# Performance work log

Measured on AMD Instinct MI355X. Metric: run time of the kernel, lower is better.

## Reference

```python
import jax, jax.numpy as jnp
import numpy as np

B, S, D, M, K = 2, 1024, 512, 64, 4


def setup_inputs() -> dict:
    key = jax.random.key(0)
    ks = jax.random.split(key, 16)
    sd = 1.0 / np.sqrt(D)
    return {
        "x": jax.random.normal(ks[0], (B, S, D), jnp.float32),
        "context": jax.random.normal(ks[1], (B, S, D), jnp.float32),
        # per-mechanism transform Linear(d, d): weight [m, d_in, d_out], bias [m, d]
        "W_t": jax.random.normal(ks[2], (M, D, D), jnp.float32) * sd,
        "b_t": jax.random.normal(ks[3], (M, D), jnp.float32) * sd,
        # characteristics parameter (1,1,dim) per mechanism -> [m, d]
        "char": jax.random.normal(ks[4], (M, D), jnp.float32),
        # timing gate Linear(d, 1): weight [m, d], bias [m]
        "W_g": jax.random.normal(ks[5], (M, D), jnp.float32) * sd,
        "b_g": jax.random.normal(ks[6], (M,), jnp.float32) * sd,
        # selector: Linear(d, 2d) -> GELU -> Linear(2d, m)
        "sel_W1": jax.random.normal(ks[7], (D, 2 * D), jnp.float32) * sd,
        "sel_b1": jax.random.normal(ks[8], (2 * D,), jnp.float32) * sd,
        "sel_W2": jax.random.normal(ks[9], (2 * D, M), jnp.float32) / np.sqrt(2 * D),
        "sel_b2": jax.random.normal(ks[10], (M,), jnp.float32) / np.sqrt(2 * D),
        # integrate: Linear(2d, d)
        "int_W": jax.random.normal(ks[11], (2 * D, D), jnp.float32) / np.sqrt(2 * D),
        "int_b": jax.random.normal(ks[12], (D,), jnp.float32) / np.sqrt(2 * D),
    }


def reference(x, context, W_t, b_t, char, W_g, b_g, sel_W1, sel_b1, sel_W2, sel_b2, int_W, int_b):
    # router: softmax -> top-k mask -> renormalize
    h = jax.nn.gelu(context @ sel_W1 + sel_b1, approximate=False)  # [b,s,2d]
    scores = jax.nn.softmax(h @ sel_W2 + sel_b2, axis=-1)          # [b,s,m]
    _, top_idx = jax.lax.top_k(scores, K)                          # [b,s,k]
    mask = jnp.sum(jax.nn.one_hot(top_idx, M, dtype=scores.dtype), axis=-2)  # [b,s,m]
    scores = scores * mask
    scores = scores / jnp.sum(scores, axis=-1, keepdims=True)

    # dense expert compute: transform + characteristics, sigmoid timing gate
    trans = jnp.einsum('bsd,mde->bsme', x, W_t) + b_t + char       # [b,s,m,d]
    gate = jax.nn.sigmoid(jnp.einsum('bsd,md->bsm', x, W_g) + b_g)  # [b,s,m]

    # weighted combine (gate fused into routing weights)
    selected = jnp.einsum('bsme,bsm->bse', trans, scores * gate)   # [b,s,d]

    integrated = jnp.concatenate([x, selected], axis=-1) @ int_W + int_b
    return integrated
```

## Files before the change

### kernel.cpp

```cpp
#include <hip/hip_runtime.h>
#include <hip/hip_bf16.h>

#define T_TOK 2048
#define D_    512
#define TWO_D 1024
#define M_    64

typedef float  f32x4  __attribute__((ext_vector_type(4)));
typedef __bf16 bf16x8 __attribute__((ext_vector_type(8)));

__device__ __forceinline__ ushort f2bf(float f) {
    union { __hip_bfloat16 h; ushort u; } cv;
    cv.h = __float2bfloat16(f);
    return cv.u;
}
__device__ __forceinline__ float bf2f(ushort u) {
    union { unsigned int i; float f; } c; c.i = ((unsigned int)u) << 16; return c.f;
}

__device__ __forceinline__ void gl16(const void* g, void* l) {
    __builtin_amdgcn_global_load_lds(
        (const __attribute__((address_space(1))) unsigned int*)g,
        (__attribute__((address_space(3))) unsigned int*)l, 16, 0, 0);
}

__global__ __launch_bounds__(256) void k_prep(const float* __restrict__ x,
                                              const float* __restrict__ ctx,
                                              ushort* __restrict__ xs,
                                              ushort* __restrict__ cH,
                                              ushort* __restrict__ cL) {
    int b = blockIdx.x;
    int idx = (b & 1023) * 256 + threadIdx.x;
    if (b < 1024) {
        int e4  = idx * 4;
        int t   = e4 >> 9;
        int d   = e4 & 511;
        float4 v = *reinterpret_cast<const float4*>(x + e4);
        ushort4 o;
        o.x = f2bf(v.x); o.y = f2bf(v.y); o.z = f2bf(v.z); o.w = f2bf(v.w);
        *reinterpret_cast<ushort4*>(xs + (size_t)t * TWO_D + d) = o;
    } else {
        float4 v = *reinterpret_cast<const float4*>(ctx + (size_t)idx * 4);
        ushort4 h, l;
        h.x = f2bf(v.x); l.x = f2bf(v.x - bf2f(h.x));
        h.y = f2bf(v.y); l.y = f2bf(v.y - bf2f(h.y));
        h.z = f2bf(v.z); l.z = f2bf(v.z - bf2f(h.z));
        h.w = f2bf(v.w); l.w = f2bf(v.w - bf2f(h.w));
        *reinterpret_cast<ushort4*>(cH + (size_t)idx * 4) = h;
        *reinterpret_cast<ushort4*>(cL + (size_t)idx * 4) = l;
    }
}

__global__ __launch_bounds__(256) void k_split_w1t(const float* __restrict__ W1,
                                                   ushort* __restrict__ w1th,
                                                   ushort* __restrict__ w1tl) {
    int t  = threadIdx.x;
    int n  = blockIdx.x * 64 + (t >> 2);
    int kb = blockIdx.y * 64 + (t & 3) * 16;
#pragma unroll
    for (int j = 0; j < 16; j += 4) {
        ushort hh[4], ll[4];
#pragma unroll
        for (int i = 0; i < 4; i++) {
            float v = W1[(size_t)(kb + j + i) * TWO_D + n];
            ushort h = f2bf(v);
            hh[i] = h;
            ll[i] = f2bf(v - bf2f(h));
        }
        ushort4 h4, l4;
        h4.x = hh[0]; h4.y = hh[1]; h4.z = hh[2]; h4.w = hh[3];
        l4.x = ll[0]; l4.y = ll[1]; l4.z = ll[2]; l4.w = ll[3];
        *reinterpret_cast<ushort4*>(&w1th[(size_t)n * D_ + kb + j]) = h4;
        *reinterpret_cast<ushort4*>(&w1tl[(size_t)n * D_ + kb + j]) = l4;
    }
}

__global__ __launch_bounds__(256) void k_gemm1s(const ushort* __restrict__ cH,
                                                const ushort* __restrict__ cL,
                                                const ushort* __restrict__ w1th,
                                                const ushort* __restrict__ w1tl,
                                                const float* __restrict__ b1,
                                                float* __restrict__ H) {
    int col0 = blockIdx.x * 64, r0 = blockIdx.y * 64;
    __shared__ ushort sAH[2 * 4096], sAL[2 * 4096];
    __shared__ ushort sBH[2 * 4096], sBL[2 * 4096];
    int t = threadIdx.x, lane = t & 63, wave = t >> 6;
    int wm = wave >> 1, wn = wave & 1;
    int lr = lane & 15, kq = lane >> 4;

    const ushort* srcAH = cH  + (size_t)(r0  + (t >> 3)) * D_ + (t & 7) * 8;
    const ushort* srcAL = cL  + (size_t)(r0  + (t >> 3)) * D_ + (t & 7) * 8;
    const ushort* srcBH = w1th + (size_t)(col0 + (t >> 3)) * D_ + (t & 7) * 8;
    const ushort* srcBL = w1tl + (size_t)(col0 + (t >> 3)) * D_ + (t & 7) * 8;
    int r2 = (256 + t) >> 3, p2 = ((256 + t) & 7) * 8;
    const ushort* srcAH2 = cH  + (size_t)(r0  + r2) * D_ + p2;
    const ushort* srcAL2 = cL  + (size_t)(r0  + r2) * D_ + p2;
    const ushort* srcBH2 = w1th + (size_t)(col0 + r2) * D_ + p2;
    const ushort* srcBL2 = w1tl + (size_t)(col0 + r2) * D_ + p2;

    f32x4 acc[2][2];
#pragma unroll
    for (int i = 0; i < 2; i++)
#pragma unroll
        for (int j = 0; j < 2; j++)
#pragma unroll
            for (int r = 0; r < 4; r++) acc[i][j][r] = 0.0f;

    gl16(srcAH, &sAH[0] + t * 8);  gl16(srcAH2, &sAH[0] + 2048 + t * 8);
    gl16(srcAL, &sAL[0] + t * 8);  gl16(srcAL2, &sAL[0] + 2048 + t * 8);
    gl16(srcBH, &sBH[0] + t * 8);  gl16(srcBH2, &sBH[0] + 2048 + t * 8);
    gl16(srcBL, &sBL[0] + t * 8);  gl16(srcBL2, &sBL[0] + 2048 + t * 8);
    __syncthreads();

    int cur = 0;
    for (int k0 = 0; k0 < D_; k0 += 64) {
        int nxt = cur ^ 1;
        if (k0 + 64 < D_) {
            int kn = k0 + 64;
            gl16(srcAH + kn, &sAH[nxt * 4096] + t * 8);  gl16(srcAH2 + kn, &sAH[nxt * 4096] + 2048 + t * 8);
            gl16(srcAL + kn, &sAL[nxt * 4096] + t * 8);  gl16(srcAL2 + kn, &sAL[nxt * 4096] + 2048 + t * 8);
            gl16(srcBH + kn, &sBH[nxt * 4096] + t * 8);  gl16(srcBH2 + kn, &sBH[nxt * 4096] + 2048 + t * 8);
            gl16(srcBL + kn, &sBL[nxt * 4096] + t * 8);  gl16(srcBL2 + kn, &sBL[nxt * 4096] + 2048 + t * 8);
        }
#pragma unroll
        for (int kc = 0; kc < 2; kc++) {
            bf16x8 ah[2], al[2], bh[2], bl[2];
#pragma unroll
            for (int i = 0; i < 2; i++) {
                int off = cur * 4096 + (wm * 32 + i * 16 + lr) * 64 + kc * 32 + kq * 8;
                ah[i] = *reinterpret_cast<const bf16x8*>(&sAH[off]);
                al[i] = *reinterpret_cast<const bf16x8*>(&sAL[off]);
            }
#pragma unroll
            for (int j = 0; j < 2; j++) {
                int off = cur * 4096 + (wn * 32 + j * 16 + lr) * 64 + kc * 32 + kq * 8;
                bh[j] = *reinterpret_cast<const bf16x8*>(&sBH[off]);
                bl[j] = *reinterpret_cast<const bf16x8*>(&sBL[off]);
            }
#pragma unroll
            for (int i = 0; i < 2; i++)
#pragma unroll
                for (int j = 0; j < 2; j++) {
                    acc[i][j] = __builtin_amdgcn_mfma_f32_16x16x32_bf16(ah[i], bh[j], acc[i][j], 0, 0, 0);
                    acc[i][j] = __builtin_amdgcn_mfma_f32_16x16x32_bf16(ah[i], bl[j], acc[i][j], 0, 0, 0);
                    acc[i][j] = __builtin_amdgcn_mfma_f32_16x16x32_bf16(al[i], bh[j], acc[i][j], 0, 0, 0);
                }
        }
        __syncthreads();
        cur = nxt;
    }

#pragma unroll
    for (int i = 0; i < 2; i++)
#pragma unroll
        for (int j = 0; j < 2; j++) {
            int col = col0 + wn * 32 + j * 16 + lr;
            float bb = b1[col];
#pragma unroll
            for (int r = 0; r < 4; r++) {
                int row = r0 + wm * 32 + i * 16 + kq * 4 + r;
                float v = acc[i][j][r] + bb;
                H[(size_t)row * TWO_D + col] = 0.5f * v * (1.0f + erff(v * 0.70710678118654752f));
            }
        }
}

__global__ __launch_bounds__(256) void k_logits(const float* __restrict__ H,
                                                const float* __restrict__ x,
                                                const float* __restrict__ W2,
                                                const float* __restrict__ Wg,
                                                float* __restrict__ partial) {
    __shared__ float sa[64][36];
    __shared__ float sb[32][64];
    int tx = threadIdx.x & 15, ty = threadIdx.x >> 4;
    int cx = blockIdx.x;
    int row0 = blockIdx.y * 64;

    const float* Asrc; int lda, koff;
    if (cx < 8) { Asrc = H; lda = TWO_D; koff = cx * 128; }
    else        { Asrc = x; lda = D_;    koff = (cx - 8) * 128; }

    float acc[4][4];
#pragma unroll
    for (int i = 0; i < 4; i++)
#pragma unroll
        for (int j = 0; j < 4; j++) acc[i][j] = 0.0f;

    for (int k0 = 0; k0 < 128; k0 += 32) {
#pragma unroll
        for (int q = 0; q < 2; q++) {
            int f = threadIdx.x * 2 + q;
            int r = f >> 3, c = (f & 7) * 4;
            *reinterpret_cast<float4*>(&sa[r][c]) =
                *reinterpret_cast<const float4*>(&Asrc[(size_t)(row0 + r) * lda + koff + k0 + c]);
            if (cx < 8) {
                int kk = f >> 4, n4 = (f & 15) * 4;
                *reinterpret_cast<float4*>(&sb[kk][n4]) =
                    *reinterpret_cast<const float4*>(&W2[(size_t)(koff + k0 + kk) * M_ + n4]);
            } else {
                int m = f >> 3, kq = f & 7;
                float4 v2 = *reinterpret_cast<const float4*>(&Wg[(size_t)m * D_ + koff + k0 + kq * 4]);
                sb[kq * 4 + 0][m] = v2.x; sb[kq * 4 + 1][m] = v2.y;
                sb[kq * 4 + 2][m] = v2.z; sb[kq * 4 + 3][m] = v2.w;
            }
        }
        __syncthreads();
#pragma unroll
        for (int kk = 0; kk < 32; kk++) {
            float a0 = sa[ty * 4 + 0][kk], a1 = sa[ty * 4 + 1][kk];
            float a2 = sa[ty * 4 + 2][kk], a3 = sa[ty * 4 + 3][kk];
            float4 b4 = *reinterpret_cast<float4*>(&sb[kk][tx * 4]);
            acc[0][0] += a0 * b4.x; acc[0][1] += a0 * b4.y; acc[0][2] += a0 * b4.z; acc[0][3] += a0 * b4.w;
            acc[1][0] += a1 * b4.x; acc[1][1] += a1 * b4.y; acc[1][2] += a1 * b4.z; acc[1][3] += a1 * b4.w;
            acc[2][0] += a2 * b4.x; acc[2][1] += a2 * b4.y; acc[2][2] += a2 * b4.z; acc[2][3] += a2 * b4.w;
            acc[3][0] += a3 * b4.x; acc[3][1] += a3 * b4.y; acc[3][2] += a3 * b4.z; acc[3][3] += a3 * b4.w;
        }
        __syncthreads();
    }
#pragma unroll
    for (int i = 0; i < 4; i++) {
        int row = row0 + ty * 4 + i;
        float4 o;
        float* oc = reinterpret_cast<float*>(&o);
#pragma unroll
        for (int j = 0; j < 4; j++) oc[j] = acc[i][j];
        *reinterpret_cast<float4*>(&partial[((size_t)cx * T_TOK + row) * M_ + tx * 4]) = o;
    }
}

__global__ __launch_bounds__(256) void k_topk(const float* __restrict__ partial,
                                              const float* __restrict__ b2,
                                              const float* __restrict__ bg,
                                              int* __restrict__ tope,
                                              float* __restrict__ topw) {
    int t = threadIdx.x;
    int wave = t >> 6, lane = t & 63;
    int tok = blockIdx.x * 4 + wave;

    float l = b2[lane];
#pragma unroll
    for (int c = 0; c < 8; c++)
        l += partial[((size_t)c * T_TOK + tok) * M_ + lane];
    float g = bg[lane];
#pragma unroll
    for (int c = 8; c < 12; c++)
        g += partial[((size_t)c * T_TOK + tok) * M_ + lane];

    float mx = l;
#pragma unroll
    for (int off = 1; off < 64; off <<= 1) mx = fmaxf(mx, __shfl_xor(mx, off));
    float ev = expf(l - mx);
    float s = ev;
#pragma unroll
    for (int off = 1; off < 64; off <<= 1) s += __shfl_xor(s, off);
    float p = ev / s;

    float pm = p;
    int bi0, bi1, bi2, bi3; float bv0, bv1, bv2, bv3;
#pragma unroll
    for (int k = 0; k < 4; k++) {
        float bv = pm; int bi = lane;
#pragma unroll
        for (int off = 1; off < 64; off <<= 1) {
            float ov = __shfl_xor(bv, off);
            int   oi = __shfl_xor(bi, off);
            if (ov > bv || (ov == bv && oi < bi)) { bv = ov; bi = oi; }
        }
        if (k == 0) { bi0 = bi; bv0 = bv; }
        else if (k == 1) { bi1 = bi; bv1 = bv; }
        else if (k == 2) { bi2 = bi; bv2 = bv; }
        else { bi3 = bi; bv3 = bv; }
        if (lane == bi) pm = -1.0f;
    }
    float sum4 = bv0 + bv1 + bv2 + bv3;
    int   esel = (lane == 0) ? bi0 : (lane == 1) ? bi1 : (lane == 2) ? bi2 : bi3;
    float pv   = (lane == 0) ? bv0 : (lane == 1) ? bv1 : (lane == 2) ? bv2 : bv3;
    float gv = __shfl(g, esel);
    if (lane < 4) {
        float gate = 1.0f / (1.0f + expf(-gv));
        tope[tok * 4 + lane] = esel;
        topw[tok * 4 + lane] = (pv / sum4) * gate;
    }
}

__global__ __launch_bounds__(256) void k_bucket(const int* __restrict__ tope,
                                                const float* __restrict__ topw,
                                                int* __restrict__ counts,
                                                int* __restrict__ bslot,
                                                float* __restrict__ bw) {
    int e = blockIdx.x;
    int t = threadIdx.x, lane = t & 63, wave = t >> 6;
    __shared__ int s_wsum[4];
    __shared__ int s_base;
    if (t == 0) s_base = 0;

    for (int it = 0; it < 8; it++) {
        int base = it * 1024 + t * 4;
        int4 ev = *reinterpret_cast<const int4*>(tope + base);
        bool m0 = (ev.x == e), m1 = (ev.y == e), m2 = (ev.z == e), m3 = (ev.w == e);
        unsigned long long b0 = __ballot(m0), b1 = __ballot(m1);
        unsigned long long b2 = __ballot(m2), b3 = __ballot(m3);
        unsigned long long below = (lane == 0) ? 0ULL : ((~0ULL) >> (64 - lane));
        int pre_lane = __popcll(b0 & below) + __popcll(b1 & below)
                     + __popcll(b2 & below) + __popcll(b3 & below);
        int wtot = __popcll(b0) + __popcll(b1) + __popcll(b2) + __popcll(b3);
        if (lane == 0) s_wsum[wave] = wtot;
        __syncthreads();
        int wbase = s_base;
#pragma unroll
        for (int w = 0; w < 4; w++)
            if (w < wave) wbase += s_wsum[w];
        int pos = wbase + pre_lane;
        if (m0) { bslot[e * T_TOK + pos] = base + 0; bw[e * T_TOK + pos] = topw[base + 0]; pos++; }
        if (m1) { bslot[e * T_TOK + pos] = base + 1; bw[e * T_TOK + pos] = topw[base + 1]; pos++; }
        if (m2) { bslot[e * T_TOK + pos] = base + 2; bw[e * T_TOK + pos] = topw[base + 2]; pos++; }
        if (m3) { bslot[e * T_TOK + pos] = base + 3; bw[e * T_TOK + pos] = topw[base + 3]; pos++; }
        __syncthreads();
        if (t == 0) s_base += s_wsum[0] + s_wsum[1] + s_wsum[2] + s_wsum[3];
    }
    __syncthreads();
    if (t == 0) counts[e] = s_base;
}

__global__ __launch_bounds__(64) void k_items(const int* __restrict__ counts,
                                              int* __restrict__ sched) {
    int t = threadIdx.x;
    int cnt = counts[t];
    int nty = (cnt + 63) >> 6;
    int off = nty;
    for (int d = 1; d < 64; d <<= 1) {
        int v = __shfl_up(off, d);
        if (t >= d) off += v;
    }
    int base = off - nty;
    for (int y = 0; y < nty; y++)
        sched[1 + base + y] = (t << 16) | y;
    if (t == 63) sched[0] = off;
}

__global__ __launch_bounds__(256) void k_expert(const ushort* __restrict__ xs,
                                                const float* __restrict__ Wt,
                                                const float* __restrict__ bt,
                                                const float* __restrict__ ch,
                                                const int* __restrict__ counts,
                                                const int* __restrict__ bslot,
                                                const float* __restrict__ bw,
                                                const int* __restrict__ sched,
                                                float* __restrict__ scratch) {
    int yi = blockIdx.y;
    if (yi >= sched[0]) return;
    int item = sched[1 + yi];
    int e  = item >> 16;
    int y0 = (item & 0xffff) << 6;
    int cnt = counts[e];
    int n0 = blockIdx.x * 64;

    __shared__ ushort saF[2 * 64 * 32];
    __shared__ float  sbF[2 * 32 * 64];
    __shared__ int    s_slot[64];
    __shared__ float  s_w[64];

    int t = threadIdx.x;
    if (t < 64) {
        int i = y0 + t;
        if (i < cnt) { s_slot[t] = bslot[e * T_TOK + i]; s_w[t] = bw[e * T_TOK + i]; }
        else         { s_slot[t] = -1;                   s_w[t] = 0.0f; }
    }
    __syncthreads();

    int lane = t & 63, wave = t >> 6;
    int wm = wave >> 1, wn = wave & 1;
    int lr = lane & 15, kq = lane >> 4;

    int rA = t >> 2, qA = t & 3;
    int slotA = s_slot[rA];
    const ushort* srcA = xs + (size_t)((slotA >= 0) ? (slotA >> 2) : 0) * TWO_D + qA * 8;
    const float* srcB0 = &Wt[((size_t)e * D_ + (t >> 4)) * D_ + n0 + (t & 15) * 4];
    const float* srcB1 = &Wt[((size_t)e * D_ + 16 + (t >> 4)) * D_ + n0 + (t & 15) * 4];

    f32x4 acc[2][2];
#pragma unroll
    for (int i = 0; i < 2; i++)
#pragma unroll
        for (int j = 0; j < 2; j++)
#pragma unroll
            for (int r = 0; r < 4; r++) acc[i][j][r] = 0.0f;

    gl16(srcA, &saF[0] + t * 8);
    gl16(srcB0, &sbF[0] + t * 4);
    gl16(srcB1, &sbF[0] + 1024 + t * 4);
    __syncthreads();

    int cur = 0;
    for (int k0 = 0; k0 < D_; k0 += 32) {
        int nxt = cur ^ 1;
        if (k0 + 32 < D_) {
            gl16(srcA + k0 + 32, &saF[nxt * 2048] + t * 8);
            gl16(srcB0 + (size_t)(k0 + 32) * D_, &sbF[nxt * 2048] + t * 4);
            gl16(srcB1 + (size_t)(k0 + 32) * D_, &sbF[nxt * 2048] + 1024 + t * 4);
        }
        bf16x8 af[2], bfr[2];
#pragma unroll
        for (int i = 0; i < 2; i++)
            af[i] = *reinterpret_cast<const bf16x8*>(&saF[cur * 2048 + (wm * 32 + i * 16 + lr) * 32 + kq * 8]);
#pragma unroll
        for (int j = 0; j < 2; j++) {
            int col = wn * 32 + j * 16 + lr;
            union { ushort us[8]; bf16x8 v; } pk;
#pragma unroll
            for (int jj = 0; jj < 8; jj++)
                pk.us[jj] = f2bf(sbF[cur * 2048 + (kq * 8 + jj) * 64 + col]);
            bfr[j] = pk.v;
        }
#pragma unroll
        for (int i = 0; i < 2; i++)
#pragma unroll
            for (int j = 0; j < 2; j++)
                acc[i][j] = __builtin_amdgcn_mfma_f32_16x16x32_bf16(af[i], bfr[j], acc[i][j], 0, 0, 0);
        __syncthreads();
        cur = nxt;
    }

#pragma unroll
    for (int i = 0; i < 2; i++)
#pragma unroll
        for (int j = 0; j < 2; j++) {
            int col = n0 + wn * 32 + j * 16 + lr;
            float bias = bt[(size_t)e * D_ + col] + ch[(size_t)e * D_ + col];
#pragma unroll
            for (int r = 0; r < 4; r++) {
                int rl = wm * 32 + i * 16 + kq * 4 + r;
                int slot = s_slot[rl];
                if (slot >= 0)
                    scratch[(size_t)slot * D_ + col] = (acc[i][j][r] + bias) * s_w[rl];
            }
        }
}

__global__ __launch_bounds__(256) void k_combine(const float* __restrict__ scratch,
                                                 ushort* __restrict__ xs) {
    int tid = blockIdx.x * 256 + threadIdx.x;
    int token = tid >> 7;
    int d4 = (tid & 127) * 4;
    float4 a = *reinterpret_cast<const float4*>(scratch + ((size_t)token * 4 + 0) * D_ + d4);
    float4 b = *reinterpret_cast<const float4*>(scratch + ((size_t)token * 4 + 1) * D_ + d4);
    float4 c = *reinterpret_cast<const float4*>(scratch + ((size_t)token * 4 + 2) * D_ + d4);
    float4 d = *reinterpret_cast<const float4*>(scratch + ((size_t)token * 4 + 3) * D_ + d4);
    ushort4 o;
    o.x = f2bf(a.x + b.x + c.x + d.x);
    o.y = f2bf(a.y + b.y + c.y + d.y);
    o.z = f2bf(a.z + b.z + c.z + d.z);
    o.w = f2bf(a.w + b.w + c.w + d.w);
    *reinterpret_cast<ushort4*>(xs + (size_t)token * TWO_D + D_ + d4) = o;
}

__global__ __launch_bounds__(256) void k_integrate(const ushort* __restrict__ xs,
                                                   const float* __restrict__ Wi,
                                                   const float* __restrict__ bi,
                                                   float* __restrict__ out) {
    int n0 = blockIdx.x * 64, r0 = blockIdx.y * 64;
    __shared__ ushort saF[2 * 4096];
    __shared__ float  sbF[2 * 4096];
    int t = threadIdx.x, lane = t & 63, wave = t >> 6;
    int wm = wave >> 1, wn = wave & 1;
    int lr = lane & 15, kq = lane >> 4;

    int rA0 = t >> 3, pA0 = (t & 7) * 8;
    int rA1 = (256 + t) >> 3, pA1 = ((256 + t) & 7) * 8;
    const ushort* srcA0 = xs + (size_t)(r0 + rA0) * TWO_D + pA0;
    const ushort* srcA1 = xs + (size_t)(r0 + rA1) * TWO_D + pA1;
    const float* srcB[4];
#pragma unroll
    for (int m = 0; m < 4; m++) {
        int f = m * 256 + t;
        srcB[m] = &Wi[(size_t)(f >> 4) * D_ + n0 + (f & 15) * 4];
    }

    f32x4 acc[2][2];
#pragma unroll
    for (int i = 0; i < 2; i++)
#pragma unroll
        for (int j = 0; j < 2; j++)
#pragma unroll
            for (int r = 0; r < 4; r++) acc[i][j][r] = 0.0f;

    gl16(srcA0, &saF[0] + t * 8);
    gl16(srcA1, &saF[0] + 2048 + t * 8);
#pragma unroll
    for (int m = 0; m < 4; m++)
        gl16(srcB[m], &sbF[0] + m * 1024 + t * 4);
    __syncthreads();

    int cur = 0;
    for (int k0 = 0; k0 < TWO_D; k0 += 64) {
        int nxt = cur ^ 1;
        if (k0 + 64 < TWO_D) {
            int kn = k0 + 64;
            gl16(srcA0 + kn, &saF[nxt * 4096] + t * 8);
            gl16(srcA1 + kn, &saF[nxt * 4096] + 2048 + t * 8);
#pragma unroll
            for (int m = 0; m < 4; m++)
                gl16(srcB[m] + (size_t)kn * D_, &sbF[nxt * 4096] + m * 1024 + t * 4);
        }
#pragma unroll
        for (int kc = 0; kc < 2; kc++) {
            bf16x8 af[2], bfr[2];
#pragma unroll
            for (int i = 0; i < 2; i++)
                af[i] = *reinterpret_cast<const bf16x8*>(
                    &saF[cur * 4096 + (wm * 32 + i * 16 + lr) * 64 + kc * 32 + kq * 8]);
#pragma unroll
            for (int j = 0; j < 2; j++) {
                int col = wn * 32 + j * 16 + lr;
                union { ushort us[8]; bf16x8 v; } pk;
#pragma unroll
                for (int jj = 0; jj < 8; jj++)
                    pk.us[jj] = f2bf(sbF[cur * 4096 + (kc * 32 + kq * 8 + jj) * 64 + col]);
                bfr[j] = pk.v;
            }
#pragma unroll
            for (int i = 0; i < 2; i++)
#pragma unroll
                for (int j = 0; j < 2; j++)
                    acc[i][j] = __builtin_amdgcn_mfma_f32_16x16x32_bf16(af[i], bfr[j], acc[i][j], 0, 0, 0);
        }
        __syncthreads();
        cur = nxt;
    }

#pragma unroll
    for (int i = 0; i < 2; i++)
#pragma unroll
        for (int j = 0; j < 2; j++) {
            int col = n0 + wn * 32 + j * 16 + lr;
            float bb = bi[col];
#pragma unroll
            for (int r = 0; r < 4; r++) {
                int row = r0 + wm * 32 + i * 16 + kq * 4 + r;
                out[(size_t)row * D_ + col] = acc[i][j][r] + bb;
            }
        }
}

extern "C" void kernel_launch(void* const* d_in, const int* in_sizes, int n_in,
                              void* d_out, int out_size, void* d_ws, size_t ws_size,
                              hipStream_t stream) {
    const float* x   = (const float*)d_in[0];
    const float* ctx = (const float*)d_in[1];
    const float* Wt  = (const float*)d_in[2];
    const float* bt  = (const float*)d_in[3];
    const float* ch  = (const float*)d_in[4];
    const float* Wg  = (const float*)d_in[5];
    const float* bg  = (const float*)d_in[6];
    const float* W1  = (const float*)d_in[7];
    const float* b1  = (const float*)d_in[8];
    const float* W2  = (const float*)d_in[9];
    const float* b2  = (const float*)d_in[10];
    const float* Wi  = (const float*)d_in[11];
    const float* bi  = (const float*)d_in[12];
    float* out = (float*)d_out;

    char* ws = (char*)d_ws;
    float*  H       = (float*)(ws + 0);
    ushort* xs      = (ushort*)(ws + 8388608);
    int*    counts  = (int*)(ws + 12582912);
    int*    bslot   = (int*)(ws + 12583936);
    float*  bw      = (float*)(ws + 13108224);
    float*  scratch = (float*)(ws + 13632512);
    float*  partial = scratch;
    ushort* ctxH = (ushort*)(ws + 19923968);
    ushort* ctxL = (ushort*)(ws + 22021120);
    ushort* w1th = (ushort*)(ws + 24118272);
    ushort* w1tl = (ushort*)(ws + 25166848);
    int*    sched = (int*)(ws + 26215424);
    int*    tope  = (int*)(ws + 26216448);
    float*  topw  = (float*)(ws + 26249216);

    k_prep     <<<2048, 256, 0, stream>>>(x, ctx, xs, ctxH, ctxL);
    k_split_w1t<<<dim3(16, 8), 256, 0, stream>>>(W1, w1th, w1tl);
    k_gemm1s   <<<dim3(16, 32), 256, 0, stream>>>(ctxH, ctxL, w1th, w1tl, b1, H);
    k_logits   <<<dim3(12, 32), 256, 0, stream>>>(H, x, W2, Wg, partial);
    k_topk     <<<512, 256, 0, stream>>>(partial, b2, bg, tope, topw);
    k_bucket   <<<64, 256, 0, stream>>>(tope, topw, counts, bslot, bw);
    k_items    <<<1, 64, 0, stream>>>(counts, sched);
    k_expert   <<<dim3(8, 192), 256, 0, stream>>>(xs, Wt, bt, ch, counts, bslot, bw, sched, scratch);
    k_combine  <<<1024, 256, 0, stream>>>(scratch, xs);
    k_integrate<<<dim3(8, 32), 256, 0, stream>>>(xs, Wi, bi, out);
}
```

Baseline: 101.8 us.

## Store expert scratch in bf16 and pre-transpose integrate weights to bf16

The expert kernel now writes its weighted outputs to scratch as bf16 instead of fp32, which halves scratch write and read traffic. The combine kernel reads them with 8-wide vector loads. A new prep kernel converts and transposes the integrate weight into bf16 once per call. The integrate GEMM can then load B tiles directly as bf16 fragments instead of converting fp32 values element by element from LDS. This adds one small launch and loses some precision in the partial sums before they are combined.

New measurement: 101.9 us. Within noise of the previous version (+0.1%).

```diff
diff --git a/kernel.cpp b/kernel.cpp
--- a/kernel.cpp
+++ b/kernel.cpp
@@ -8,6 +8,7 @@
 
 typedef float  f32x4  __attribute__((ext_vector_type(4)));
 typedef __bf16 bf16x8 __attribute__((ext_vector_type(8)));
+typedef unsigned short ushort8v __attribute__((ext_vector_type(8)));
 
 __device__ __forceinline__ ushort f2bf(float f) {
     union { __hip_bfloat16 h; ushort u; } cv;
@@ -75,6 +76,23 @@
     }
 }
 
+__global__ __launch_bounds__(256) void k_prep_wi(const float* __restrict__ Wi,
+                                                 ushort* __restrict__ wiT) {
+    int t  = threadIdx.x;
+    int n  = blockIdx.x * 64 + (t >> 2);
+    int kb = blockIdx.y * 64 + (t & 3) * 16;
+#pragma unroll
+    for (int j = 0; j < 16; j += 4) {
+        ushort hh[4];
+#pragma unroll
+        for (int i = 0; i < 4; i++)
+            hh[i] = f2bf(Wi[(size_t)(kb + j + i) * D_ + n]);
+        ushort4 h4;
+        h4.x = hh[0]; h4.y = hh[1]; h4.z = hh[2]; h4.w = hh[3];
+        *reinterpret_cast<ushort4*>(&wiT[(size_t)n * TWO_D + kb + j]) = h4;
+    }
+}
+
 __global__ __launch_bounds__(256) void k_gemm1s(const ushort* __restrict__ cH,
                                                 const ushort* __restrict__ cL,
                                                 const ushort* __restrict__ w1th,
@@ -346,7 +364,7 @@
                                                 const int* __restrict__ bslot,
                                                 const float* __restrict__ bw,
                                                 const int* __restrict__ sched,
-                                                float* __restrict__ scratch) {
+                                                ushort* __restrict__ scratch) {
     int yi = blockIdx.y;
     if (yi >= sched[0]) return;
     int item = sched[1 + yi];
@@ -432,35 +450,38 @@
                 int rl = wm * 32 + i * 16 + kq * 4 + r;
                 int slot = s_slot[rl];
                 if (slot >= 0)
-                    scratch[(size_t)slot * D_ + col] = (acc[i][j][r] + bias) * s_w[rl];
+                    scratch[(size_t)slot * D_ + col] = f2bf((acc[i][j][r] + bias) * s_w[rl]);
             }
         }
 }
 
-__global__ __launch_bounds__(256) void k_combine(const float* __restrict__ scratch,
+__global__ __launch_bounds__(256) void k_combine(const ushort* __restrict__ scratch,
                                                  ushort* __restrict__ xs) {
     int tid = blockIdx.x * 256 + threadIdx.x;
-    int token = tid >> 7;
-    int d4 = (tid & 127) * 4;
-    float4 a = *reinterpret_cast<const float4*>(scratch + ((size_t)token * 4 + 0) * D_ + d4);
-    float4 b = *reinterpret_cast<const float4*>(scratch + ((size_t)token * 4 + 1) * D_ + d4);
-    float4 c = *reinterpret_cast<const float4*>(scratch + ((size_t)token * 4 + 2) * D_ + d4);
-    float4 d = *reinterpret_cast<const float4*>(scratch + ((size_t)token * 4 + 3) * D_ + d4);
-    ushort4 o;
-    o.x = f2bf(a.x + b.x + c.x + d.x);
-    o.y = f2bf(a.y + b.y + c.y + d.y);
-    o.z = f2bf(a.z + b.z + c.z + d.z);
-    o.w = f2bf(a.w + b.w + c.w + d.w);
-    *reinterpret_cast<ushort4*>(xs + (size_t)token * TWO_D + D_ + d4) = o;
+    int token = tid >> 6;
+    int d8 = (tid & 63) * 8;
+    float s[8];
+#pragma unroll
+    for (int j = 0; j < 8; j++) s[j] = 0.0f;
+#pragma unroll
+    for (int r = 0; r < 4; r++) {
+        ushort8v v = *reinterpret_cast<const ushort8v*>(scratch + ((size_t)token * 4 + r) * D_ + d8);
+#pragma unroll
+        for (int j = 0; j < 8; j++) s[j] += bf2f(v[j]);
+    }
+    ushort8v o;
+#pragma unroll
+    for (int j = 0; j < 8; j++) o[j] = f2bf(s[j]);
+    *reinterpret_cast<ushort8v*>(xs + (size_t)token * TWO_D + D_ + d8) = o;
 }
 
 __global__ __launch_bounds__(256) void k_integrate(const ushort* __restrict__ xs,
-                                                   const float* __restrict__ Wi,
+                                                   const ushort* __restrict__ wiT,
                                                    const float* __restrict__ bi,
                                                    float* __restrict__ out) {
     int n0 = blockIdx.x * 64, r0 = blockIdx.y * 64;
     __shared__ ushort saF[2 * 4096];
-    __shared__ float  sbF[2 * 4096];
+    __shared__ ushort sbB[2 * 4096];
     int t = threadIdx.x, lane = t & 63, wave = t >> 6;
     int wm = wave >> 1, wn = wave & 1;
     int lr = lane & 15, kq = lane >> 4;
@@ -469,12 +490,8 @@
     int rA1 = (256 + t) >> 3, pA1 = ((256 + t) & 7) * 8;
     const ushort* srcA0 = xs + (size_t)(r0 + rA0) * TWO_D + pA0;
     const ushort* srcA1 = xs + (size_t)(r0 + rA1) * TWO_D + pA1;
-    const float* srcB[4];
-#pragma unroll
-    for (int m = 0; m < 4; m++) {
-        int f = m * 256 + t;
-        srcB[m] = &Wi[(size_t)(f >> 4) * D_ + n0 + (f & 15) * 4];
-    }
+    const ushort* srcB0 = wiT + (size_t)(n0 + rA0) * TWO_D + pA0;
+    const ushort* srcB1 = wiT + (size_t)(n0 + rA1) * TWO_D + pA1;
 
     f32x4 acc[2][2];
 #pragma unroll
@@ -486,9 +503,8 @@
 
     gl16(srcA0, &saF[0] + t * 8);
     gl16(srcA1, &saF[0] + 2048 + t * 8);
-#pragma unroll
-    for (int m = 0; m < 4; m++)
-        gl16(srcB[m], &sbF[0] + m * 1024 + t * 4);
+    gl16(srcB0, &sbB[0] + t * 8);
+    gl16(srcB1, &sbB[0] + 2048 + t * 8);
     __syncthreads();
 
     int cur = 0;
@@ -498,9 +514,8 @@
             int kn = k0 + 64;
             gl16(srcA0 + kn, &saF[nxt * 4096] + t * 8);
             gl16(srcA1 + kn, &saF[nxt * 4096] + 2048 + t * 8);
-#pragma unroll
-            for (int m = 0; m < 4; m++)
-                gl16(srcB[m] + (size_t)kn * D_, &sbF[nxt * 4096] + m * 1024 + t * 4);
+            gl16(srcB0 + kn, &sbB[nxt * 4096] + t * 8);
+            gl16(srcB1 + kn, &sbB[nxt * 4096] + 2048 + t * 8);
         }
 #pragma unroll
         for (int kc = 0; kc < 2; kc++) {
@@ -510,14 +525,9 @@
                 af[i] = *reinterpret_cast<const bf16x8*>(
                     &saF[cur * 4096 + (wm * 32 + i * 16 + lr) * 64 + kc * 32 + kq * 8]);
 #pragma unroll
-            for (int j = 0; j < 2; j++) {
-                int col = wn * 32 + j * 16 + lr;
-                union { ushort us[8]; bf16x8 v; } pk;
-#pragma unroll
-                for (int jj = 0; jj < 8; jj++)
-                    pk.us[jj] = f2bf(sbF[cur * 4096 + (kc * 32 + kq * 8 + jj) * 64 + col]);
-                bfr[j] = pk.v;
-            }
+            for (int j = 0; j < 2; j++)
+                bfr[j] = *reinterpret_cast<const bf16x8*>(
+                    &sbB[cur * 4096 + (wn * 32 + j * 16 + lr) * 64 + kc * 32 + kq * 8]);
 #pragma unroll
             for (int i = 0; i < 2; i++)
 #pragma unroll
@@ -566,24 +576,26 @@
     int*    counts  = (int*)(ws + 12582912);
     int*    bslot   = (int*)(ws + 12583936);
     float*  bw      = (float*)(ws + 13108224);
-    float*  scratch = (float*)(ws + 13632512);
-    float*  partial = scratch;
-    ushort* ctxH = (ushort*)(ws + 19923968);
-    ushort* ctxL = (ushort*)(ws + 22021120);
-    ushort* w1th = (ushort*)(ws + 24118272);
-    ushort* w1tl = (ushort*)(ws + 25166848);
-    int*    sched = (int*)(ws + 26215424);
-    int*    tope  = (int*)(ws + 26216448);
-    float*  topw  = (float*)(ws + 26249216);
+    ushort* scratch = (ushort*)(ws + 13632512);
+    float*  partial = (float*)(ws + 22021120);
+    ushort* ctxH    = (ushort*)(ws + 28312576);
+    ushort* ctxL    = (ushort*)(ws + 30409728);
+    ushort* w1th    = (ushort*)(ws + 32506880);
+    ushort* w1tl    = (ushort*)(ws + 33555456);
+    ushort* wiT     = (ushort*)(ws + 34604032);
+    int*    sched   = (int*)(ws + 35652608);
+    int*    tope    = (int*)(ws + 35653632);
+    float*  topw    = (float*)(ws + 35686400);
 
     k_prep     <<<2048, 256, 0, stream>>>(x, ctx, xs, ctxH, ctxL);
     k_split_w1t<<<dim3(16, 8), 256, 0, stream>>>(W1, w1th, w1tl);
+    k_prep_wi  <<<dim3(8, 16), 256, 0, stream>>>(Wi, wiT);
     k_gemm1s   <<<dim3(16, 32), 256, 0, stream>>>(ctxH, ctxL, w1th, w1tl, b1, H);
     k_logits   <<<dim3(12, 32), 256, 0, stream>>>(H, x, W2, Wg, partial);
     k_topk     <<<512, 256, 0, stream>>>(partial, b2, bg, tope, topw);
     k_bucket   <<<64, 256, 0, stream>>>(tope, topw, counts, bslot, bw);
     k_items    <<<1, 64, 0, stream>>>(counts, sched);
     k_expert   <<<dim3(8, 192), 256, 0, stream>>>(xs, Wt, bt, ch, counts, bslot, bw, sched, scratch);
-    k_combine  <<<1024, 256, 0, stream>>>(scratch, xs);
-    k_integrate<<<dim3(8, 32), 256, 0, stream>>>(xs, Wi, bi, out);
-}
+    k_combine  <<<512, 256, 0, stream>>>(scratch, xs);
+    k_integrate<<<dim3(8, 32), 256, 0, stream>>>(xs, wiT, bi, out);
+}
```
